# Kernel tuning notes

Hardware: AMD Instinct MI355X
Metric: run time of the kernel (lower is better)

The kernel has to match this reference:

```python
import jax, jax.numpy as jnp
import numpy as np

CROP = 20
HALF = CROP // 2  # also the zero-padding width
HID = 128
NCLS = 10
B = 16384


def setup_inputs() -> dict:
    key = jax.random.key(0)
    ks = jax.random.split(key, 16)
    s = 0.05
    inp = {
        "image": jax.random.uniform(ks[0], (B, 1, 28, 28), dtype=jnp.float32),
        # centers in padded coordinates, kept in-bounds: [HALF, 48-HALF]
        "center": jax.random.randint(ks[1], (B, 2), HALF, 48 - HALF + 1, dtype=jnp.int64),
        "h0": jax.random.normal(ks[2], (2, B, HID), dtype=jnp.float32),
        # RNN layer 0 (input 400 -> 128)
        "W_ih0": jax.random.normal(ks[3], (HID, CROP * CROP), dtype=jnp.float32) * s,
        "b_ih0": jax.random.normal(ks[4], (HID,), dtype=jnp.float32) * s,
        "W_hh0": jax.random.normal(ks[5], (HID, HID), dtype=jnp.float32) * s,
        "b_hh0": jax.random.normal(ks[6], (HID,), dtype=jnp.float32) * s,
        # RNN layer 1 (128 -> 128)
        "W_ih1": jax.random.normal(ks[7], (HID, HID), dtype=jnp.float32) * s,
        "b_ih1": jax.random.normal(ks[8], (HID,), dtype=jnp.float32) * s,
        "W_hh1": jax.random.normal(ks[9], (HID, HID), dtype=jnp.float32) * s,
        "b_hh1": jax.random.normal(ks[10], (HID,), dtype=jnp.float32) * s,
        # heads
        "W_cls": jax.random.normal(ks[11], (NCLS, HID), dtype=jnp.float32) * s,
        "b_cls": jax.random.normal(ks[12], (NCLS,), dtype=jnp.float32) * s,
        "W_act": jax.random.normal(ks[13], (2, HID), dtype=jnp.float32) * s,
        "b_act": jax.random.normal(ks[14], (2,), dtype=jnp.float32) * s,
    }
    return inp


def _crop(padded, center):
    # padded: (B,1,P,P), center: (B,2) with (x, y) in padded coords
    b = padded.shape[0]
    r = jnp.arange(CROP)
    ys = (center[:, 1] - HALF)[:, None] + r  # (B, CROP)
    xs = (center[:, 0] - HALF)[:, None] + r  # (B, CROP)
    bi = jnp.arange(b)[:, None, None]
    return padded[bi, 0, ys[:, :, None], xs[:, None, :]]  # (B, CROP, CROP)


def reference(image, center, h0,
              W_ih0, b_ih0, W_hh0, b_hh0,
              W_ih1, b_ih1, W_hh1, b_hh1,
              W_cls, b_cls, W_act, b_act):
    b = image.shape[0]
    padded = jnp.pad(image, ((0, 0), (0, 0), (HALF, HALF), (HALF, HALF)))
    x = _crop(padded, center).reshape(b, -1)  # (B, 400)
    # single-step, 2-layer tanh RNN
    h1 = jnp.tanh(x @ W_ih0.T + b_ih0 + h0[0] @ W_hh0.T + b_hh0)
    h2 = jnp.tanh(h1 @ W_ih1.T + b_ih1 + h0[1] @ W_hh1.T + b_hh1)
    hn = jnp.stack([h1, h2])  # (2, B, HID)
    class_pred = h2 @ W_cls.T + b_cls
    action_pred = h2 @ W_act.T + b_act
    return class_pred, action_pred, hn
```

## Files before the change

### kernel.cpp

```cpp
#include <hip/hip_runtime.h>
#include <hip/hip_bf16.h>

#define B_TOT 16384
#define MTILE 16

typedef __bf16 bf16x8 __attribute__((ext_vector_type(8)));
typedef float  f32x4  __attribute__((ext_vector_type(4)));

#define NG0 (17*8*64)
#define NG1 (8*8*64)
#define NGH (4*64)
#define WP0_OFF  0
#define WP1_OFF  (NG0*16)
#define WPH_OFF  (WP1_OFF + NG1*16)
#define BIAS0_OFF (WPH_OFF + NGH*16)
#define BIAS1_OFF (BIAS0_OFF + 512)
#define BIASH_OFF (BIAS1_OFF + 512)
#define ZERO_OFF  (BIASH_OFF + 512)
#define PREP_BLOCKS 53

__device__ __forceinline__ float fast_tanh(float x) {
    float cx = fminf(fmaxf(x, -9.f), 9.f);
    float t = __builtin_amdgcn_exp2f(cx * 2.8853900817779268f);
    return 1.f - 2.f * __builtin_amdgcn_rcpf(t + 1.f);
}

__device__ __forceinline__ void gl_lds4(const float* g, void* l) {
    __builtin_amdgcn_global_load_lds((const __attribute__((address_space(1))) void*)g,
                                     (__attribute__((address_space(3))) void*)l, 4, 0, 0);
}
__device__ __forceinline__ void gl_lds16(const float* g, void* l) {
    __builtin_amdgcn_global_load_lds((const __attribute__((address_space(1))) void*)g,
                                     (__attribute__((address_space(3))) void*)l, 16, 0, 0);
}

__device__ __forceinline__ bf16x8 cvt8(f32x4 a, f32x4 b) {
    bf16x8 v;
    v[0]=(__bf16)a.x; v[1]=(__bf16)a.y; v[2]=(__bf16)a.z; v[3]=(__bf16)a.w;
    v[4]=(__bf16)b.x; v[5]=(__bf16)b.y; v[6]=(__bf16)b.z; v[7]=(__bf16)b.w;
    return v;
}

__global__ __launch_bounds__(256) void prepack_kernel(
    const float* __restrict__ Wih0, const float* __restrict__ Whh0,
    const float* __restrict__ Wih1, const float* __restrict__ Whh1,
    const float* __restrict__ Wcls, const float* __restrict__ Wact,
    const float* __restrict__ bih0, const float* __restrict__ bhh0,
    const float* __restrict__ bih1, const float* __restrict__ bhh1,
    const float* __restrict__ bcls, const float* __restrict__ bact,
    char* __restrict__ ws)
{
    int idx = blockIdx.x * 256 + threadIdx.x;
    __bf16* wp0 = (__bf16*)(ws + WP0_OFF);
    __bf16* wp1 = (__bf16*)(ws + WP1_OFF);
    __bf16* wph = (__bf16*)(ws + WPH_OFF);
    float* bias0 = (float*)(ws + BIAS0_OFF);
    float* bias1 = (float*)(ws + BIAS1_OFF);
    float* biash = (float*)(ws + BIASH_OFF);

    if (idx < NG0) {
        int lane = idx & 63, g = idx >> 6, s = g >> 3, nb = g & 7;
        int n = nb * 16 + (lane & 15);
        int kb = s * 32 + (lane >> 4) * 8;
        bf16x8 v;
        #pragma unroll
        for (int j = 0; j < 8; ++j) {
            int k = kb + j;
            float x = 0.f;
            if (k < 400)       x = Wih0[n * 400 + k];
            else if (k >= 416) x = Whh0[n * 128 + (k - 416)];
            v[j] = (__bf16)x;
        }
        *(bf16x8*)(wp0 + (size_t)idx * 8) = v;
    } else if (idx < NG0 + NG1) {
        int i2 = idx - NG0;
        int lane = i2 & 63, g = i2 >> 6, s = g >> 3, nb = g & 7;
        int n = nb * 16 + (lane & 15);
        int kb = s * 32 + (lane >> 4) * 8;
        bf16x8 v;
        #pragma unroll
        for (int j = 0; j < 8; ++j) {
            int k = kb + j;
            float x = (k < 128) ? Wih1[n * 128 + k] : Whh1[n * 128 + (k - 128)];
            v[j] = (__bf16)x;
        }
        *(bf16x8*)(wp1 + (size_t)i2 * 8) = v;
    } else if (idx < NG0 + NG1 + NGH) {
        int i3 = idx - NG0 - NG1;
        int lane = i3 & 63, s = i3 >> 6;
        int n = lane & 15;
        int kb = s * 32 + (lane >> 4) * 8;
        bf16x8 v;
        #pragma unroll
        for (int j = 0; j < 8; ++j) {
            int k = kb + j;
            float x = 0.f;
            if (n < 10)      x = Wcls[n * 128 + k];
            else if (n < 12) x = Wact[(n - 10) * 128 + k];
            v[j] = (__bf16)x;
        }
        *(bf16x8*)(wph + (size_t)i3 * 8) = v;
    } else {
        int i4 = idx - NG0 - NG1 - NGH;
        if (i4 < 128) bias0[i4] = bih0[i4] + bhh0[i4];
        else if (i4 < 256) { int i = i4 - 128; bias1[i] = bih1[i] + bhh1[i]; }
        else if (i4 < 272) {
            int i = i4 - 256;
            biash[i] = (i < 10) ? bcls[i] : ((i < 12) ? bact[i - 10] : 0.f);
        } else if (i4 < 336) {
            ((float*)(ws + ZERO_OFF))[i4 - 272] = 0.f;
        }
    }
}

#define STGSTR 452
#define HEXSTR 136

__global__ __launch_bounds__(256) void fused_main(
    const float* __restrict__ image, const int* __restrict__ center,
    const float* __restrict__ h0, const char* __restrict__ ws,
    float* __restrict__ out)
{
    const bf16x8* wp0 = (const bf16x8*)(ws + WP0_OFF);
    const bf16x8* wp1 = (const bf16x8*)(ws + WP1_OFF);
    const bf16x8* wph = (const bf16x8*)(ws + WPH_OFF);
    const float* bias0 = (const float*)(ws + BIAS0_OFF);
    const float* bias1 = (const float*)(ws + BIAS1_OFF);
    const float* biash = (const float*)(ws + BIASH_OFF);
    const float* zbuf  = (const float*)(ws + ZERO_OFF);

    __shared__ __align__(16) float stage[MTILE * STGSTR];
    __shared__ __align__(16) float h0st[16 * 256];
    __shared__ __align__(16) __bf16 h1ex[MTILE * HEXSTR];
    __bf16* h2ex = (__bf16*)stage;

    const int t = threadIdx.x, lane = t & 63, wn = t >> 6;
    const int m0 = blockIdx.x * MTILE;
    const int l15 = lane & 15, l16 = lane >> 4;

    #pragma unroll
    for (int u = 0; u < 4; ++u) {
        int c = wn * 4 + u;
        int L = c >> 3, s = (c >> 1) & 3, half = c & 1;
        const float* src = h0 + (size_t)L * B_TOT * 128
                         + (size_t)(m0 + l15) * 128 + s * 32 + l16 * 8 + half * 4;
        gl_lds16(src, &h0st[c * 256]);
    }

    const int s0 = wn * 4;
    int cxv[4], cyv[4];
    #pragma unroll
    for (int i = 0; i < 4; ++i) {
        cxv[i] = center[(m0 + s0 + i) * 2 + 0];
        cyv[i] = center[(m0 + s0 + i) * 2 + 1];
    }

    {
        int k = lane;
        int r = k / 20, c = k - r * 20;
        #pragma unroll
        for (int j = 0; j < 7; ++j) {
            #pragma unroll
            for (int i = 0; i < 4; ++i) {
                int iy = cyv[i] - 20 + r;
                int ix = cxv[i] - 20 + c;
                bool ok = ((unsigned)iy < 28u) && ((unsigned)ix < 28u) && (k < 400);
                const float* src = ok ? (image + (size_t)(m0 + s0 + i) * 784 + iy * 28 + ix)
                                      : zbuf;
                gl_lds4(src, &stage[(s0 + i) * STGSTR + j * 64]);
            }
            k += 64;
            c += 4; if (c >= 20) { c -= 20; r += 4; } else { r += 3; }
        }
    }
    __syncthreads();

    const int cg = wn;
    const int qr = l16, lr = l15;
    const float* stg = stage + lr * STGSTR;

    float* outh1 = out + (size_t)B_TOT * 12;
    float* outh2 = out + (size_t)B_TOT * 140;

    f32x4 acc0[2] = {};
    #pragma unroll
    for (int s = 0; s < 13; ++s) {
        f32x4 fa = *(const f32x4*)(stg + s * 32 + qr * 8);
        f32x4 fb = *(const f32x4*)(stg + s * 32 + qr * 8 + 4);
        bf16x8 a = cvt8(fa, fb);
        bf16x8 b0 = wp0[(size_t)(s * 8 + cg * 2 + 0) * 64 + lane];
        bf16x8 b1 = wp0[(size_t)(s * 8 + cg * 2 + 1) * 64 + lane];
        acc0[0] = __builtin_amdgcn_mfma_f32_16x16x32_bf16(a, b0, acc0[0], 0, 0, 0);
        acc0[1] = __builtin_amdgcn_mfma_f32_16x16x32_bf16(a, b1, acc0[1], 0, 0, 0);
    }
    #pragma unroll
    for (int s = 0; s < 4; ++s) {
        f32x4 fa = *(const f32x4*)(h0st + (s * 2 + 0) * 256 + lane * 4);
        f32x4 fb = *(const f32x4*)(h0st + (s * 2 + 1) * 256 + lane * 4);
        bf16x8 a = cvt8(fa, fb);
        bf16x8 b0 = wp0[(size_t)((13 + s) * 8 + cg * 2 + 0) * 64 + lane];
        bf16x8 b1 = wp0[(size_t)((13 + s) * 8 + cg * 2 + 1) * 64 + lane];
        acc0[0] = __builtin_amdgcn_mfma_f32_16x16x32_bf16(a, b0, acc0[0], 0, 0, 0);
        acc0[1] = __builtin_amdgcn_mfma_f32_16x16x32_bf16(a, b1, acc0[1], 0, 0, 0);
    }
    #pragma unroll
    for (int f = 0; f < 2; ++f) {
        int n = cg * 32 + f * 16 + lr;
        float bv = bias0[n];
        #pragma unroll
        for (int r = 0; r < 4; ++r)
            h1ex[(qr * 4 + r) * HEXSTR + n] = (__bf16)fast_tanh(acc0[f][r] + bv);
    }

    f32x4 acc1[2] = {};
    #pragma unroll
    for (int s = 0; s < 4; ++s) {
        f32x4 fa = *(const f32x4*)(h0st + (8 + s * 2 + 0) * 256 + lane * 4);
        f32x4 fb = *(const f32x4*)(h0st + (8 + s * 2 + 1) * 256 + lane * 4);
        bf16x8 a = cvt8(fa, fb);
        bf16x8 b0 = wp1[(size_t)((4 + s) * 8 + cg * 2 + 0) * 64 + lane];
        bf16x8 b1 = wp1[(size_t)((4 + s) * 8 + cg * 2 + 1) * 64 + lane];
        acc1[0] = __builtin_amdgcn_mfma_f32_16x16x32_bf16(a, b0, acc1[0], 0, 0, 0);
        acc1[1] = __builtin_amdgcn_mfma_f32_16x16x32_bf16(a, b1, acc1[1], 0, 0, 0);
    }
    __syncthreads();

    {
        int row = t >> 4, c0 = (t & 15) * 8;
        bf16x8 hv = *(const bf16x8*)(h1ex + row * HEXSTR + c0);
        float4 o1, o2;
        o1.x=(float)hv[0]; o1.y=(float)hv[1]; o1.z=(float)hv[2]; o1.w=(float)hv[3];
        o2.x=(float)hv[4]; o2.y=(float)hv[5]; o2.z=(float)hv[6]; o2.w=(float)hv[7];
        *(float4*)(outh1 + (size_t)(m0 + row) * 128 + c0) = o1;
        *(float4*)(outh1 + (size_t)(m0 + row) * 128 + c0 + 4) = o2;
    }

    {
        const __bf16* h1row = h1ex + lr * HEXSTR + qr * 8;
        #pragma unroll
        for (int s = 0; s < 4; ++s) {
            bf16x8 a  = *(const bf16x8*)(h1row + s * 32);
            bf16x8 b0 = wp1[(size_t)(s * 8 + cg * 2 + 0) * 64 + lane];
            bf16x8 b1 = wp1[(size_t)(s * 8 + cg * 2 + 1) * 64 + lane];
            acc1[0] = __builtin_amdgcn_mfma_f32_16x16x32_bf16(a, b0, acc1[0], 0, 0, 0);
            acc1[1] = __builtin_amdgcn_mfma_f32_16x16x32_bf16(a, b1, acc1[1], 0, 0, 0);
        }
    }
    #pragma unroll
    for (int f = 0; f < 2; ++f) {
        int n = cg * 32 + f * 16 + lr;
        float bv = bias1[n];
        #pragma unroll
        for (int r = 0; r < 4; ++r)
            h2ex[(qr * 4 + r) * HEXSTR + n] = (__bf16)fast_tanh(acc1[f][r] + bv);
    }
    __syncthreads();

    {
        int row = t >> 4, c0 = (t & 15) * 8;
        bf16x8 hv = *(const bf16x8*)(h2ex + row * HEXSTR + c0);
        float4 o1, o2;
        o1.x=(float)hv[0]; o1.y=(float)hv[1]; o1.z=(float)hv[2]; o1.w=(float)hv[3];
        o2.x=(float)hv[4]; o2.y=(float)hv[5]; o2.z=(float)hv[6]; o2.w=(float)hv[7];
        *(float4*)(outh2 + (size_t)(m0 + row) * 128 + c0) = o1;
        *(float4*)(outh2 + (size_t)(m0 + row) * 128 + c0 + 4) = o2;
    }

    if (cg == 0) {
        f32x4 acc2 = {};
        const __bf16* h2row = h2ex + lr * HEXSTR + qr * 8;
        #pragma unroll
        for (int s = 0; s < 4; ++s) {
            bf16x8 a = *(const bf16x8*)(h2row + s * 32);
            bf16x8 b = wph[(size_t)s * 64 + lane];
            acc2 = __builtin_amdgcn_mfma_f32_16x16x32_bf16(a, b, acc2, 0, 0, 0);
        }
        float bhd = biash[lr];
        #pragma unroll
        for (int r = 0; r < 4; ++r) {
            int mg = m0 + qr * 4 + r;
            float v = acc2[r] + bhd;
            if (lr < 10)      out[(size_t)mg * 10 + lr] = v;
            else if (lr < 12) out[(size_t)B_TOT * 10 + (size_t)mg * 2 + (lr - 10)] = v;
        }
    }
}

extern "C" void kernel_launch(void* const* d_in, const int* in_sizes, int n_in,
                              void* d_out, int out_size, void* d_ws, size_t ws_size,
                              hipStream_t stream) {
    const float* image = (const float*)d_in[0];
    const int*   center = (const int*)d_in[1];
    const float* h0   = (const float*)d_in[2];
    const float* Wih0 = (const float*)d_in[3];
    const float* bih0 = (const float*)d_in[4];
    const float* Whh0 = (const float*)d_in[5];
    const float* bhh0 = (const float*)d_in[6];
    const float* Wih1 = (const float*)d_in[7];
    const float* bih1 = (const float*)d_in[8];
    const float* Whh1 = (const float*)d_in[9];
    const float* bhh1 = (const float*)d_in[10];
    const float* Wcls = (const float*)d_in[11];
    const float* bcls = (const float*)d_in[12];
    const float* Wact = (const float*)d_in[13];
    const float* bact = (const float*)d_in[14];

    prepack_kernel<<<PREP_BLOCKS, 256, 0, stream>>>(
        Wih0, Whh0, Wih1, Whh1, Wcls, Wact,
        bih0, bhh0, bih1, bhh1, bcls, bact, (char*)d_ws);
    fused_main<<<B_TOT / MTILE, 256, 0, stream>>>(
        image, center, h0, (const char*)d_ws, (float*)d_out);
}
```

Before: 29.08 us.

## Load contiguous image row band with 16B LDS DMA, then crop in LDS

Replaces the per-element 4-byte global-to-LDS gather of crop pixels with 16-byte loads of a contiguous 20-row band of each image into LDS. A second pass crops from that band, zero-pads and converts to bf16 in shared memory, so the MFMA loop reads bf16 directly. The h1/h2 outputs are now written in fp32 straight from the tanh results instead of via a bf16 LDS round trip, and the layer-1 h0 load is deferred to reuse LDS. This cuts the number of load instructions but adds an extra LDS pass, a barrier, and uncoalesced scalar output stores.

```diff
diff --git a/kernel.cpp b/kernel.cpp
--- a/kernel.cpp
+++ b/kernel.cpp
@@ -16,7 +16,6 @@
 #define BIAS0_OFF (WPH_OFF + NGH*16)
 #define BIAS1_OFF (BIAS0_OFF + 512)
 #define BIASH_OFF (BIAS1_OFF + 512)
-#define ZERO_OFF  (BIASH_OFF + 512)
 #define PREP_BLOCKS 53
 
 __device__ __forceinline__ float fast_tanh(float x) {
@@ -25,11 +24,7 @@
     return 1.f - 2.f * __builtin_amdgcn_rcpf(t + 1.f);
 }
 
-__device__ __forceinline__ void gl_lds4(const float* g, void* l) {
-    __builtin_amdgcn_global_load_lds((const __attribute__((address_space(1))) void*)g,
-                                     (__attribute__((address_space(3))) void*)l, 4, 0, 0);
-}
-__device__ __forceinline__ void gl_lds16(const float* g, void* l) {
+__device__ __forceinline__ void gl_lds16(const void* g, void* l) {
     __builtin_amdgcn_global_load_lds((const __attribute__((address_space(1))) void*)g,
                                      (__attribute__((address_space(3))) void*)l, 16, 0, 0);
 }
@@ -107,13 +102,12 @@
         else if (i4 < 272) {
             int i = i4 - 256;
             biash[i] = (i < 10) ? bcls[i] : ((i < 12) ? bact[i - 10] : 0.f);
-        } else if (i4 < 336) {
-            ((float*)(ws + ZERO_OFF))[i4 - 272] = 0.f;
-        }
-    }
-}
-
-#define STGSTR 452
+        }
+    }
+}
+
+#define RAWW  560
+#define XLSTR 424
 #define HEXSTR 136
 
 __global__ __launch_bounds__(256) void fused_main(
@@ -127,71 +121,107 @@
     const float* bias0 = (const float*)(ws + BIAS0_OFF);
     const float* bias1 = (const float*)(ws + BIAS1_OFF);
     const float* biash = (const float*)(ws + BIASH_OFF);
-    const float* zbuf  = (const float*)(ws + ZERO_OFF);
-
-    __shared__ __align__(16) float stage[MTILE * STGSTR];
-    __shared__ __align__(16) float h0st[16 * 256];
-    __shared__ __align__(16) __bf16 h1ex[MTILE * HEXSTR];
-    __bf16* h2ex = (__bf16*)stage;
+
+    __shared__ __align__(16) float raw[MTILE * RAWW];
+    __shared__ __align__(16) __bf16 stage[MTILE * XLSTR];
+    __shared__ __align__(16) float h0st[8 * 256];
+    __bf16* h1ex = (__bf16*)raw;
+    __bf16* h2ex = (__bf16*)(raw + 2048);
+    float*  h0st1 = raw + 4096;
 
     const int t = threadIdx.x, lane = t & 63, wn = t >> 6;
     const int m0 = blockIdx.x * MTILE;
     const int l15 = lane & 15, l16 = lane >> 4;
 
     #pragma unroll
-    for (int u = 0; u < 4; ++u) {
-        int c = wn * 4 + u;
-        int L = c >> 3, s = (c >> 1) & 3, half = c & 1;
-        const float* src = h0 + (size_t)L * B_TOT * 128
+    for (int u = 0; u < 2; ++u) {
+        int c = wn * 2 + u;
+        int s = c >> 1, half = c & 1;
+        const float* src = h0 + (size_t)(m0 + l15) * 128 + s * 32 + l16 * 8 + half * 4;
+        gl_lds16(src, &h0st[c * 256]);
+    }
+
+    {
+        unsigned basel = lane * 16u;
+        #pragma unroll
+        for (int j = 0; j < 9; ++j) {
+            int ii = wn + j * 4;
+            if (ii < 35) {
+                unsigned off = (unsigned)ii * 1024u + basel;
+                unsigned sm = off / 2240u;
+                unsigned within = off - sm * 2240u;
+                int cyl = center[(m0 + sm) * 2 + 1];
+                int rst = min(max(cyl - 20, 0), 8);
+                const char* src = (const char*)image
+                                + (size_t)(m0 + sm) * 3136 + (size_t)rst * 112 + within;
+                gl_lds16(src, (char*)raw + (size_t)ii * 1024);
+            }
+        }
+    }
+    __syncthreads();
+
+    {
+        int m = t >> 4, sub = t & 15;
+        int cyv = center[(m0 + m) * 2 + 1];
+        int cxv = center[(m0 + m) * 2 + 0];
+        int rst = min(max(cyv - 20, 0), 8);
+        const float* rawm = raw + m * RAWW;
+        __bf16* stm = stage + m * XLSTR;
+        #pragma unroll
+        for (int i = 0; i < 14; ++i) {
+            int k2 = (sub + i * 16) * 2;
+            if (k2 < XLSTR) {
+                float v0 = 0.f, v1 = 0.f;
+                if (k2 < 400) {
+                    int r0 = k2 / 20, c0 = k2 - r0 * 20;
+                    int iy = cyv - 20 + r0, ix = cxv - 20 + c0;
+                    bool ok = ((unsigned)iy < 28u) && ((unsigned)ix < 28u);
+                    int idx = ok ? ((iy - rst) * 28 + ix) : 0;
+                    float vv = rawm[idx];
+                    v0 = ok ? vv : 0.f;
+                    int k1 = k2 + 1;
+                    if (k1 < 400) {
+                        int r1 = (c0 == 19) ? r0 + 1 : r0;
+                        int c1 = (c0 == 19) ? 0 : c0 + 1;
+                        int iy1 = cyv - 20 + r1, ix1 = cxv - 20 + c1;
+                        bool ok1 = ((unsigned)iy1 < 28u) && ((unsigned)ix1 < 28u);
+                        int idx1 = ok1 ? ((iy1 - rst) * 28 + ix1) : 0;
+                        float vv1 = rawm[idx1];
+                        v1 = ok1 ? vv1 : 0.f;
+                    }
+                }
+                union { __bf16 b[2]; unsigned u; } p;
+                p.b[0] = (__bf16)v0; p.b[1] = (__bf16)v1;
+                *(unsigned*)(stm + k2) = p.u;
+            }
+        }
+    }
+    __syncthreads();
+
+    #pragma unroll
+    for (int u = 0; u < 2; ++u) {
+        int c = wn * 2 + u;
+        int s = c >> 1, half = c & 1;
+        const float* src = h0 + (size_t)B_TOT * 128
                          + (size_t)(m0 + l15) * 128 + s * 32 + l16 * 8 + half * 4;
-        gl_lds16(src, &h0st[c * 256]);
-    }
-
-    const int s0 = wn * 4;
-    int cxv[4], cyv[4];
-    #pragma unroll
-    for (int i = 0; i < 4; ++i) {
-        cxv[i] = center[(m0 + s0 + i) * 2 + 0];
-        cyv[i] = center[(m0 + s0 + i) * 2 + 1];
-    }
-
-    {
-        int k = lane;
-        int r = k / 20, c = k - r * 20;
-        #pragma unroll
-        for (int j = 0; j < 7; ++j) {
-            #pragma unroll
-            for (int i = 0; i < 4; ++i) {
-                int iy = cyv[i] - 20 + r;
-                int ix = cxv[i] - 20 + c;
-                bool ok = ((unsigned)iy < 28u) && ((unsigned)ix < 28u) && (k < 400);
-                const float* src = ok ? (image + (size_t)(m0 + s0 + i) * 784 + iy * 28 + ix)
-                                      : zbuf;
-                gl_lds4(src, &stage[(s0 + i) * STGSTR + j * 64]);
-            }
-            k += 64;
-            c += 4; if (c >= 20) { c -= 20; r += 4; } else { r += 3; }
-        }
-    }
-    __syncthreads();
-
-    const int cg = wn;
-    const int qr = l16, lr = l15;
-    const float* stg = stage + lr * STGSTR;
-
+        gl_lds16(src, &h0st1[c * 256]);
+    }
+
+    const int cg = wn, qr = l16, lr = l15;
     float* outh1 = out + (size_t)B_TOT * 12;
     float* outh2 = out + (size_t)B_TOT * 140;
 
     f32x4 acc0[2] = {};
-    #pragma unroll
-    for (int s = 0; s < 13; ++s) {
-        f32x4 fa = *(const f32x4*)(stg + s * 32 + qr * 8);
-        f32x4 fb = *(const f32x4*)(stg + s * 32 + qr * 8 + 4);
-        bf16x8 a = cvt8(fa, fb);
-        bf16x8 b0 = wp0[(size_t)(s * 8 + cg * 2 + 0) * 64 + lane];
-        bf16x8 b1 = wp0[(size_t)(s * 8 + cg * 2 + 1) * 64 + lane];
-        acc0[0] = __builtin_amdgcn_mfma_f32_16x16x32_bf16(a, b0, acc0[0], 0, 0, 0);
-        acc0[1] = __builtin_amdgcn_mfma_f32_16x16x32_bf16(a, b1, acc0[1], 0, 0, 0);
+    {
+        const __bf16* stg = stage + lr * XLSTR + qr * 8;
+        #pragma unroll
+        for (int s = 0; s < 13; ++s) {
+            bf16x8 a = *(const bf16x8*)(stg + s * 32);
+            bf16x8 b0 = wp0[(size_t)(s * 8 + cg * 2 + 0) * 64 + lane];
+            bf16x8 b1 = wp0[(size_t)(s * 8 + cg * 2 + 1) * 64 + lane];
+            acc0[0] = __builtin_amdgcn_mfma_f32_16x16x32_bf16(a, b0, acc0[0], 0, 0, 0);
+            acc0[1] = __builtin_amdgcn_mfma_f32_16x16x32_bf16(a, b1, acc0[1], 0, 0, 0);
+        }
     }
     #pragma unroll
     for (int s = 0; s < 4; ++s) {
@@ -208,33 +238,16 @@
         int n = cg * 32 + f * 16 + lr;
         float bv = bias0[n];
         #pragma unroll
-        for (int r = 0; r < 4; ++r)
-            h1ex[(qr * 4 + r) * HEXSTR + n] = (__bf16)fast_tanh(acc0[f][r] + bv);
-    }
+        for (int r = 0; r < 4; ++r) {
+            int ml = qr * 4 + r;
+            float hv = fast_tanh(acc0[f][r] + bv);
+            outh1[(size_t)(m0 + ml) * 128 + n] = hv;
+            h1ex[ml * HEXSTR + n] = (__bf16)hv;
+        }
+    }
+    __syncthreads();
 
     f32x4 acc1[2] = {};
-    #pragma unroll
-    for (int s = 0; s < 4; ++s) {
-        f32x4 fa = *(const f32x4*)(h0st + (8 + s * 2 + 0) * 256 + lane * 4);
-        f32x4 fb = *(const f32x4*)(h0st + (8 + s * 2 + 1) * 256 + lane * 4);
-        bf16x8 a = cvt8(fa, fb);
-        bf16x8 b0 = wp1[(size_t)((4 + s) * 8 + cg * 2 + 0) * 64 + lane];
-        bf16x8 b1 = wp1[(size_t)((4 + s) * 8 + cg * 2 + 1) * 64 + lane];
-        acc1[0] = __builtin_amdgcn_mfma_f32_16x16x32_bf16(a, b0, acc1[0], 0, 0, 0);
-        acc1[1] = __builtin_amdgcn_mfma_f32_16x16x32_bf16(a, b1, acc1[1], 0, 0, 0);
-    }
-    __syncthreads();
-
-    {
-        int row = t >> 4, c0 = (t & 15) * 8;
-        bf16x8 hv = *(const bf16x8*)(h1ex + row * HEXSTR + c0);
-        float4 o1, o2;
-        o1.x=(float)hv[0]; o1.y=(float)hv[1]; o1.z=(float)hv[2]; o1.w=(float)hv[3];
-        o2.x=(float)hv[4]; o2.y=(float)hv[5]; o2.z=(float)hv[6]; o2.w=(float)hv[7];
-        *(float4*)(outh1 + (size_t)(m0 + row) * 128 + c0) = o1;
-        *(float4*)(outh1 + (size_t)(m0 + row) * 128 + c0 + 4) = o2;
-    }
-
     {
         const __bf16* h1row = h1ex + lr * HEXSTR + qr * 8;
         #pragma unroll
@@ -247,24 +260,28 @@
         }
     }
     #pragma unroll
+    for (int s = 0; s < 4; ++s) {
+        f32x4 fa = *(const f32x4*)(h0st1 + (s * 2 + 0) * 256 + lane * 4);
+        f32x4 fb = *(const f32x4*)(h0st1 + (s * 2 + 1) * 256 + lane * 4);
+        bf16x8 a = cvt8(fa, fb);
+        bf16x8 b0 = wp1[(size_t)((4 + s) * 8 + cg * 2 + 0) * 64 + lane];
+        bf16x8 b1 = wp1[(size_t)((4 + s) * 8 + cg * 2 + 1) * 64 + lane];
+        acc1[0] = __builtin_amdgcn_mfma_f32_16x16x32_bf16(a, b0, acc1[0], 0, 0, 0);
+        acc1[1] = __builtin_amdgcn_mfma_f32_16x16x32_bf16(a, b1, acc1[1], 0, 0, 0);
+    }
+    #pragma unroll
     for (int f = 0; f < 2; ++f) {
         int n = cg * 32 + f * 16 + lr;
         float bv = bias1[n];
         #pragma unroll
-        for (int r = 0; r < 4; ++r)
-            h2ex[(qr * 4 + r) * HEXSTR + n] = (__bf16)fast_tanh(acc1[f][r] + bv);
+        for (int r = 0; r < 4; ++r) {
+            int ml = qr * 4 + r;
+            float hv = fast_tanh(acc1[f][r] + bv);
+            outh2[(size_t)(m0 + ml) * 128 + n] = hv;
+            h2ex[ml * HEXSTR + n] = (__bf16)hv;
+        }
     }
     __syncthreads();
-
-    {
-        int row = t >> 4, c0 = (t & 15) * 8;
-        bf16x8 hv = *(const bf16x8*)(h2ex + row * HEXSTR + c0);
-        float4 o1, o2;
-        o1.x=(float)hv[0]; o1.y=(float)hv[1]; o1.z=(float)hv[2]; o1.w=(float)hv[3];
-        o2.x=(float)hv[4]; o2.y=(float)hv[5]; o2.z=(float)hv[6]; o2.w=(float)hv[7];
-        *(float4*)(outh2 + (size_t)(m0 + row) * 128 + c0) = o1;
-        *(float4*)(outh2 + (size_t)(m0 + row) * 128 + c0 + 4) = o2;
-    }
 
     if (cg == 0) {
         f32x4 acc2 = {};
```

Result: slower. 33.24 us (+14.3%).

## Load h0 directly from global and write hidden states straight from MFMA registers

Applied to the files above, without the earlier changes.

Drops the LDS staging buffer for h0. Each lane now loads its h0 fragment from global memory just before the recurrent MFMAs. The bf16 round-trip through LDS for the h1/h2 output stores is replaced by scattered fp32 stores straight from the tanh results. This cuts LDS footprint, so more blocks may fit per CU, and outputs keep full fp32 precision instead of bf16-rounded values. The cost is uncoalesced scalar global stores with a 16-element column stride, and h0 global-load latency that is no longer hidden behind the crop loads.

```diff
diff --git a/kernel.cpp b/kernel.cpp
--- a/kernel.cpp
+++ b/kernel.cpp
@@ -28,10 +28,6 @@
 __device__ __forceinline__ void gl_lds4(const float* g, void* l) {
     __builtin_amdgcn_global_load_lds((const __attribute__((address_space(1))) void*)g,
                                      (__attribute__((address_space(3))) void*)l, 4, 0, 0);
-}
-__device__ __forceinline__ void gl_lds16(const float* g, void* l) {
-    __builtin_amdgcn_global_load_lds((const __attribute__((address_space(1))) void*)g,
-                                     (__attribute__((address_space(3))) void*)l, 16, 0, 0);
 }
 
 __device__ __forceinline__ bf16x8 cvt8(f32x4 a, f32x4 b) {
@@ -130,22 +126,12 @@
     const float* zbuf  = (const float*)(ws + ZERO_OFF);
 
     __shared__ __align__(16) float stage[MTILE * STGSTR];
-    __shared__ __align__(16) float h0st[16 * 256];
     __shared__ __align__(16) __bf16 h1ex[MTILE * HEXSTR];
     __bf16* h2ex = (__bf16*)stage;
 
     const int t = threadIdx.x, lane = t & 63, wn = t >> 6;
     const int m0 = blockIdx.x * MTILE;
     const int l15 = lane & 15, l16 = lane >> 4;
-
-    #pragma unroll
-    for (int u = 0; u < 4; ++u) {
-        int c = wn * 4 + u;
-        int L = c >> 3, s = (c >> 1) & 3, half = c & 1;
-        const float* src = h0 + (size_t)L * B_TOT * 128
-                         + (size_t)(m0 + l15) * 128 + s * 32 + l16 * 8 + half * 4;
-        gl_lds16(src, &h0st[c * 256]);
-    }
 
     const int s0 = wn * 4;
     int cxv[4], cyv[4];
@@ -178,6 +164,8 @@
     const int cg = wn;
     const int qr = l16, lr = l15;
     const float* stg = stage + lr * STGSTR;
+    const float* h0r0 = h0 + (size_t)(m0 + lr) * 128 + qr * 8;
+    const float* h0r1 = h0r0 + (size_t)B_TOT * 128;
 
     float* outh1 = out + (size_t)B_TOT * 12;
     float* outh2 = out + (size_t)B_TOT * 140;
@@ -195,8 +183,8 @@
     }
     #pragma unroll
     for (int s = 0; s < 4; ++s) {
-        f32x4 fa = *(const f32x4*)(h0st + (s * 2 + 0) * 256 + lane * 4);
-        f32x4 fb = *(const f32x4*)(h0st + (s * 2 + 1) * 256 + lane * 4);
+        f32x4 fa = *(const f32x4*)(h0r0 + s * 32);
+        f32x4 fb = *(const f32x4*)(h0r0 + s * 32 + 4);
         bf16x8 a = cvt8(fa, fb);
         bf16x8 b0 = wp0[(size_t)((13 + s) * 8 + cg * 2 + 0) * 64 + lane];
         bf16x8 b1 = wp0[(size_t)((13 + s) * 8 + cg * 2 + 1) * 64 + lane];
@@ -208,15 +196,19 @@
         int n = cg * 32 + f * 16 + lr;
         float bv = bias0[n];
         #pragma unroll
-        for (int r = 0; r < 4; ++r)
-            h1ex[(qr * 4 + r) * HEXSTR + n] = (__bf16)fast_tanh(acc0[f][r] + bv);
+        for (int r = 0; r < 4; ++r) {
+            int ml = qr * 4 + r;
+            float hv = fast_tanh(acc0[f][r] + bv);
+            outh1[(size_t)(m0 + ml) * 128 + n] = hv;
+            h1ex[ml * HEXSTR + n] = (__bf16)hv;
+        }
     }
 
     f32x4 acc1[2] = {};
     #pragma unroll
     for (int s = 0; s < 4; ++s) {
-        f32x4 fa = *(const f32x4*)(h0st + (8 + s * 2 + 0) * 256 + lane * 4);
-        f32x4 fb = *(const f32x4*)(h0st + (8 + s * 2 + 1) * 256 + lane * 4);
+        f32x4 fa = *(const f32x4*)(h0r1 + s * 32);
+        f32x4 fb = *(const f32x4*)(h0r1 + s * 32 + 4);
         bf16x8 a = cvt8(fa, fb);
         bf16x8 b0 = wp1[(size_t)((4 + s) * 8 + cg * 2 + 0) * 64 + lane];
         bf16x8 b1 = wp1[(size_t)((4 + s) * 8 + cg * 2 + 1) * 64 + lane];
@@ -224,16 +216,6 @@
         acc1[1] = __builtin_amdgcn_mfma_f32_16x16x32_bf16(a, b1, acc1[1], 0, 0, 0);
     }
     __syncthreads();
-
-    {
-        int row = t >> 4, c0 = (t & 15) * 8;
-        bf16x8 hv = *(const bf16x8*)(h1ex + row * HEXSTR + c0);
-        float4 o1, o2;
-        o1.x=(float)hv[0]; o1.y=(float)hv[1]; o1.z=(float)hv[2]; o1.w=(float)hv[3];
-        o2.x=(float)hv[4]; o2.y=(float)hv[5]; o2.z=(float)hv[6]; o2.w=(float)hv[7];
-        *(float4*)(outh1 + (size_t)(m0 + row) * 128 + c0) = o1;
-        *(float4*)(outh1 + (size_t)(m0 + row) * 128 + c0 + 4) = o2;
-    }
 
     {
         const __bf16* h1row = h1ex + lr * HEXSTR + qr * 8;
@@ -251,20 +233,14 @@
         int n = cg * 32 + f * 16 + lr;
         float bv = bias1[n];
         #pragma unroll
-        for (int r = 0; r < 4; ++r)
-            h2ex[(qr * 4 + r) * HEXSTR + n] = (__bf16)fast_tanh(acc1[f][r] + bv);
+        for (int r = 0; r < 4; ++r) {
+            int ml = qr * 4 + r;
+            float hv = fast_tanh(acc1[f][r] + bv);
+            outh2[(size_t)(m0 + ml) * 128 + n] = hv;
+            h2ex[ml * HEXSTR + n] = (__bf16)hv;
+        }
     }
     __syncthreads();
-
-    {
-        int row = t >> 4, c0 = (t & 15) * 8;
-        bf16x8 hv = *(const bf16x8*)(h2ex + row * HEXSTR + c0);
-        float4 o1, o2;
-        o1.x=(float)hv[0]; o1.y=(float)hv[1]; o1.z=(float)hv[2]; o1.w=(float)hv[3];
-        o2.x=(float)hv[4]; o2.y=(float)hv[5]; o2.z=(float)hv[6]; o2.w=(float)hv[7];
-        *(float4*)(outh2 + (size_t)(m0 + row) * 128 + c0) = o1;
-        *(float4*)(outh2 + (size_t)(m0 + row) * 128 + c0 + 4) = o2;
-    }
 
     if (cg == 0) {
         f32x4 acc2 = {};
```

Result: slower. 32.22 us (+10.8%).

## Stream weight fragments through per-wave LDS ring with async global-to-LDS loads

Applied to the files above, without the earlier changes.

Weight fragments that were loaded straight from global memory into registers are now prefetched into a per-wave 6-slot LDS ring using global_load_lds. Explicit vmcnt/lgkmcnt waits keep four fragments in flight ahead of the MFMA chain. The aim is to hide weight-load latency behind the matrix math. Biases are also loaded early, and the h1 and h2 output stores are merged after a single barrier, which delays the h1 writeback. The hand-written waitcnt and sched barriers constrain the compiler's scheduling, and the ring adds LDS use that may lower occupancy.

```diff
diff --git a/kernel.cpp b/kernel.cpp
--- a/kernel.cpp
+++ b/kernel.cpp
@@ -29,7 +29,7 @@
     __builtin_amdgcn_global_load_lds((const __attribute__((address_space(1))) void*)g,
                                      (__attribute__((address_space(3))) void*)l, 4, 0, 0);
 }
-__device__ __forceinline__ void gl_lds16(const float* g, void* l) {
+__device__ __forceinline__ void gl_lds16(const void* g, void* l) {
     __builtin_amdgcn_global_load_lds((const __attribute__((address_space(1))) void*)g,
                                      (__attribute__((address_space(3))) void*)l, 16, 0, 0);
 }
@@ -115,28 +115,48 @@
 
 #define STGSTR 452
 #define HEXSTR 136
+#define RSLOTS 6
+
+#define RWAIT(n) do { asm volatile("s_waitcnt vmcnt(" #n ")" ::: "memory"); \
+                      __builtin_amdgcn_sched_barrier(0); } while (0)
+#define LFENCE   do { asm volatile("s_waitcnt lgkmcnt(0)" ::: "memory"); \
+                      __builtin_amdgcn_sched_barrier(0); } while (0)
+
+__device__ __forceinline__ void issue_fi(int fi, const char* wp0b, const char* wp1b,
+                                         int cg, char* ringw, int lane) {
+    int s = fi >> 1, half = fi & 1;
+    int frag; const char* base;
+    if (s < 17)      { base = wp0b; frag = s * 8 + cg * 2 + half; }
+    else if (s < 21) { base = wp1b; frag = (4 + (s - 17)) * 8 + cg * 2 + half; }
+    else             { base = wp1b; frag = (s - 21) * 8 + cg * 2 + half; }
+    gl_lds16(base + (size_t)frag * 1024 + (size_t)lane * 16,
+             ringw + (size_t)(fi % RSLOTS) * 1024);
+}
 
 __global__ __launch_bounds__(256) void fused_main(
     const float* __restrict__ image, const int* __restrict__ center,
     const float* __restrict__ h0, const char* __restrict__ ws,
     float* __restrict__ out)
 {
-    const bf16x8* wp0 = (const bf16x8*)(ws + WP0_OFF);
-    const bf16x8* wp1 = (const bf16x8*)(ws + WP1_OFF);
-    const bf16x8* wph = (const bf16x8*)(ws + WPH_OFF);
     const float* bias0 = (const float*)(ws + BIAS0_OFF);
     const float* bias1 = (const float*)(ws + BIAS1_OFF);
     const float* biash = (const float*)(ws + BIASH_OFF);
     const float* zbuf  = (const float*)(ws + ZERO_OFF);
+    const char* wp0b = ws + WP0_OFF;
+    const char* wp1b = ws + WP1_OFF;
+    const bf16x8* wph = (const bf16x8*)(ws + WPH_OFF);
 
     __shared__ __align__(16) float stage[MTILE * STGSTR];
     __shared__ __align__(16) float h0st[16 * 256];
     __shared__ __align__(16) __bf16 h1ex[MTILE * HEXSTR];
+    __shared__ __align__(16) __bf16 ringb[4 * RSLOTS * 512];
     __bf16* h2ex = (__bf16*)stage;
 
     const int t = threadIdx.x, lane = t & 63, wn = t >> 6;
     const int m0 = blockIdx.x * MTILE;
     const int l15 = lane & 15, l16 = lane >> 4;
+    const int cg = wn, qr = l16, lr = l15;
+    char* ringw = (char*)ringb + (size_t)wn * (RSLOTS * 1024);
 
     #pragma unroll
     for (int u = 0; u < 4; ++u) {
@@ -154,6 +174,8 @@
         cxv[i] = center[(m0 + s0 + i) * 2 + 0];
         cyv[i] = center[(m0 + s0 + i) * 2 + 1];
     }
+    const float bv00 = bias0[cg * 32 + lr],      bv01 = bias0[cg * 32 + 16 + lr];
+    const float bv10 = bias1[cg * 32 + lr],      bv11 = bias1[cg * 32 + 16 + lr];
 
     {
         int k = lane;
@@ -175,95 +197,134 @@
     }
     __syncthreads();
 
-    const int cg = wn;
-    const int qr = l16, lr = l15;
     const float* stg = stage + lr * STGSTR;
+    f32x4 acc0[2] = {}, acc1[2] = {};
+
+    issue_fi(0, wp0b, wp1b, cg, ringw, lane);
+    issue_fi(1, wp0b, wp1b, cg, ringw, lane);
+    issue_fi(2, wp0b, wp1b, cg, ringw, lane);
+    issue_fi(3, wp0b, wp1b, cg, ringw, lane);
+
+    #pragma unroll
+    for (int s = 0; s < 13; ++s) {
+        RWAIT(2);
+        f32x4 fa = *(const f32x4*)(stg + s * 32 + qr * 8);
+        f32x4 fb = *(const f32x4*)(stg + s * 32 + qr * 8 + 4);
+        bf16x8 b0 = *(const bf16x8*)(ringw + (size_t)((2 * s) % RSLOTS) * 1024 + (size_t)lane * 16);
+        bf16x8 b1 = *(const bf16x8*)(ringw + (size_t)((2 * s + 1) % RSLOTS) * 1024 + (size_t)lane * 16);
+        LFENCE;
+        issue_fi(2 * s + 4, wp0b, wp1b, cg, ringw, lane);
+        issue_fi(2 * s + 5, wp0b, wp1b, cg, ringw, lane);
+        bf16x8 a = cvt8(fa, fb);
+        acc0[0] = __builtin_amdgcn_mfma_f32_16x16x32_bf16(a, b0, acc0[0], 0, 0, 0);
+        acc0[1] = __builtin_amdgcn_mfma_f32_16x16x32_bf16(a, b1, acc0[1], 0, 0, 0);
+    }
+    #pragma unroll
+    for (int u = 0; u < 4; ++u) {
+        const int s = 13 + u;
+        RWAIT(2);
+        f32x4 fa = *(const f32x4*)(h0st + (u * 2 + 0) * 256 + lane * 4);
+        f32x4 fb = *(const f32x4*)(h0st + (u * 2 + 1) * 256 + lane * 4);
+        bf16x8 b0 = *(const bf16x8*)(ringw + (size_t)((2 * s) % RSLOTS) * 1024 + (size_t)lane * 16);
+        bf16x8 b1 = *(const bf16x8*)(ringw + (size_t)((2 * s + 1) % RSLOTS) * 1024 + (size_t)lane * 16);
+        LFENCE;
+        issue_fi(2 * s + 4, wp0b, wp1b, cg, ringw, lane);
+        issue_fi(2 * s + 5, wp0b, wp1b, cg, ringw, lane);
+        bf16x8 a = cvt8(fa, fb);
+        acc0[0] = __builtin_amdgcn_mfma_f32_16x16x32_bf16(a, b0, acc0[0], 0, 0, 0);
+        acc0[1] = __builtin_amdgcn_mfma_f32_16x16x32_bf16(a, b1, acc0[1], 0, 0, 0);
+    }
+    #pragma unroll
+    for (int r = 0; r < 4; ++r) {
+        int ml = qr * 4 + r;
+        h1ex[ml * HEXSTR + cg * 32 + lr]      = (__bf16)fast_tanh(acc0[0][r] + bv00);
+        h1ex[ml * HEXSTR + cg * 32 + 16 + lr] = (__bf16)fast_tanh(acc0[1][r] + bv01);
+    }
+    #pragma unroll
+    for (int u = 0; u < 4; ++u) {
+        const int s = 17 + u;
+        RWAIT(2);
+        f32x4 fa = *(const f32x4*)(h0st + (8 + u * 2 + 0) * 256 + lane * 4);
+        f32x4 fb = *(const f32x4*)(h0st + (8 + u * 2 + 1) * 256 + lane * 4);
+        bf16x8 b0 = *(const bf16x8*)(ringw + (size_t)((2 * s) % RSLOTS) * 1024 + (size_t)lane * 16);
+        bf16x8 b1 = *(const bf16x8*)(ringw + (size_t)((2 * s + 1) % RSLOTS) * 1024 + (size_t)lane * 16);
+        LFENCE;
+        if (s < 20) {
+            issue_fi(2 * s + 4, wp0b, wp1b, cg, ringw, lane);
+            issue_fi(2 * s + 5, wp0b, wp1b, cg, ringw, lane);
+        } else {
+            issue_fi(44, wp0b, wp1b, cg, ringw, lane);
+            issue_fi(45, wp0b, wp1b, cg, ringw, lane);
+        }
+        bf16x8 a = cvt8(fa, fb);
+        acc1[0] = __builtin_amdgcn_mfma_f32_16x16x32_bf16(a, b0, acc1[0], 0, 0, 0);
+        acc1[1] = __builtin_amdgcn_mfma_f32_16x16x32_bf16(a, b1, acc1[1], 0, 0, 0);
+    }
+    __syncthreads();
+
+    {
+        const __bf16* h1row = h1ex + lr * HEXSTR + qr * 8;
+        {
+            bf16x8 a = *(const bf16x8*)(h1row + 0 * 32);
+            bf16x8 b0 = *(const bf16x8*)(ringw + (size_t)(42 % RSLOTS) * 1024 + (size_t)lane * 16);
+            bf16x8 b1 = *(const bf16x8*)(ringw + (size_t)(43 % RSLOTS) * 1024 + (size_t)lane * 16);
+            LFENCE;
+            issue_fi(46, wp0b, wp1b, cg, ringw, lane);
+            issue_fi(47, wp0b, wp1b, cg, ringw, lane);
+            acc1[0] = __builtin_amdgcn_mfma_f32_16x16x32_bf16(a, b0, acc1[0], 0, 0, 0);
+            acc1[1] = __builtin_amdgcn_mfma_f32_16x16x32_bf16(a, b1, acc1[1], 0, 0, 0);
+        }
+        {
+            bf16x8 a = *(const bf16x8*)(h1row + 1 * 32);
+            bf16x8 b0 = *(const bf16x8*)(ringw + (size_t)(44 % RSLOTS) * 1024 + (size_t)lane * 16);
+            bf16x8 b1 = *(const bf16x8*)(ringw + (size_t)(45 % RSLOTS) * 1024 + (size_t)lane * 16);
+            LFENCE;
+            issue_fi(48, wp0b, wp1b, cg, ringw, lane);
+            issue_fi(49, wp0b, wp1b, cg, ringw, lane);
+            acc1[0] = __builtin_amdgcn_mfma_f32_16x16x32_bf16(a, b0, acc1[0], 0, 0, 0);
+            acc1[1] = __builtin_amdgcn_mfma_f32_16x16x32_bf16(a, b1, acc1[1], 0, 0, 0);
+        }
+        RWAIT(2);
+        {
+            bf16x8 a = *(const bf16x8*)(h1row + 2 * 32);
+            bf16x8 b0 = *(const bf16x8*)(ringw + (size_t)(46 % RSLOTS) * 1024 + (size_t)lane * 16);
+            bf16x8 b1 = *(const bf16x8*)(ringw + (size_t)(47 % RSLOTS) * 1024 + (size_t)lane * 16);
+            acc1[0] = __builtin_amdgcn_mfma_f32_16x16x32_bf16(a, b0, acc1[0], 0, 0, 0);
+            acc1[1] = __builtin_amdgcn_mfma_f32_16x16x32_bf16(a, b1, acc1[1], 0, 0, 0);
+        }
+        RWAIT(0);
+        {
+            bf16x8 a = *(const bf16x8*)(h1row + 3 * 32);
+            bf16x8 b0 = *(const bf16x8*)(ringw + (size_t)(48 % RSLOTS) * 1024 + (size_t)lane * 16);
+            bf16x8 b1 = *(const bf16x8*)(ringw + (size_t)(49 % RSLOTS) * 1024 + (size_t)lane * 16);
+            acc1[0] = __builtin_amdgcn_mfma_f32_16x16x32_bf16(a, b0, acc1[0], 0, 0, 0);
+            acc1[1] = __builtin_amdgcn_mfma_f32_16x16x32_bf16(a, b1, acc1[1], 0, 0, 0);
+        }
+    }
+    #pragma unroll
+    for (int r = 0; r < 4; ++r) {
+        int ml = qr * 4 + r;
+        h2ex[ml * HEXSTR + cg * 32 + lr]      = (__bf16)fast_tanh(acc1[0][r] + bv10);
+        h2ex[ml * HEXSTR + cg * 32 + 16 + lr] = (__bf16)fast_tanh(acc1[1][r] + bv11);
+    }
+    __syncthreads();
 
     float* outh1 = out + (size_t)B_TOT * 12;
     float* outh2 = out + (size_t)B_TOT * 140;
 
-    f32x4 acc0[2] = {};
-    #pragma unroll
-    for (int s = 0; s < 13; ++s) {
-        f32x4 fa = *(const f32x4*)(stg + s * 32 + qr * 8);
-        f32x4 fb = *(const f32x4*)(stg + s * 32 + qr * 8 + 4);
-        bf16x8 a = cvt8(fa, fb);
-        bf16x8 b0 = wp0[(size_t)(s * 8 + cg * 2 + 0) * 64 + lane];
-        bf16x8 b1 = wp0[(size_t)(s * 8 + cg * 2 + 1) * 64 + lane];
-        acc0[0] = __builtin_amdgcn_mfma_f32_16x16x32_bf16(a, b0, acc0[0], 0, 0, 0);
-        acc0[1] = __builtin_amdgcn_mfma_f32_16x16x32_bf16(a, b1, acc0[1], 0, 0, 0);
-    }
-    #pragma unroll
-    for (int s = 0; s < 4; ++s) {
-        f32x4 fa = *(const f32x4*)(h0st + (s * 2 + 0) * 256 + lane * 4);
-        f32x4 fb = *(const f32x4*)(h0st + (s * 2 + 1) * 256 + lane * 4);
-        bf16x8 a = cvt8(fa, fb);
-        bf16x8 b0 = wp0[(size_t)((13 + s) * 8 + cg * 2 + 0) * 64 + lane];
-        bf16x8 b1 = wp0[(size_t)((13 + s) * 8 + cg * 2 + 1) * 64 + lane];
-        acc0[0] = __builtin_amdgcn_mfma_f32_16x16x32_bf16(a, b0, acc0[0], 0, 0, 0);
-        acc0[1] = __builtin_amdgcn_mfma_f32_16x16x32_bf16(a, b1, acc0[1], 0, 0, 0);
-    }
-    #pragma unroll
-    for (int f = 0; f < 2; ++f) {
-        int n = cg * 32 + f * 16 + lr;
-        float bv = bias0[n];
-        #pragma unroll
-        for (int r = 0; r < 4; ++r)
-            h1ex[(qr * 4 + r) * HEXSTR + n] = (__bf16)fast_tanh(acc0[f][r] + bv);
-    }
-
-    f32x4 acc1[2] = {};
-    #pragma unroll
-    for (int s = 0; s < 4; ++s) {
-        f32x4 fa = *(const f32x4*)(h0st + (8 + s * 2 + 0) * 256 + lane * 4);
-        f32x4 fb = *(const f32x4*)(h0st + (8 + s * 2 + 1) * 256 + lane * 4);
-        bf16x8 a = cvt8(fa, fb);
-        bf16x8 b0 = wp1[(size_t)((4 + s) * 8 + cg * 2 + 0) * 64 + lane];
-        bf16x8 b1 = wp1[(size_t)((4 + s) * 8 + cg * 2 + 1) * 64 + lane];
-        acc1[0] = __builtin_amdgcn_mfma_f32_16x16x32_bf16(a, b0, acc1[0], 0, 0, 0);
-        acc1[1] = __builtin_amdgcn_mfma_f32_16x16x32_bf16(a, b1, acc1[1], 0, 0, 0);
-    }
-    __syncthreads();
-
     {
         int row = t >> 4, c0 = (t & 15) * 8;
-        bf16x8 hv = *(const bf16x8*)(h1ex + row * HEXSTR + c0);
-        float4 o1, o2;
-        o1.x=(float)hv[0]; o1.y=(float)hv[1]; o1.z=(float)hv[2]; o1.w=(float)hv[3];
-        o2.x=(float)hv[4]; o2.y=(float)hv[5]; o2.z=(float)hv[6]; o2.w=(float)hv[7];
-        *(float4*)(outh1 + (size_t)(m0 + row) * 128 + c0) = o1;
+        bf16x8 hv1 = *(const bf16x8*)(h1ex + row * HEXSTR + c0);
+        bf16x8 hv2 = *(const bf16x8*)(h2ex + row * HEXSTR + c0);
+        float4 o1, o2, o3, o4;
+        o1.x=(float)hv1[0]; o1.y=(float)hv1[1]; o1.z=(float)hv1[2]; o1.w=(float)hv1[3];
+        o2.x=(float)hv1[4]; o2.y=(float)hv1[5]; o2.z=(float)hv1[6]; o2.w=(float)hv1[7];
+        o3.x=(float)hv2[0]; o3.y=(float)hv2[1]; o3.z=(float)hv2[2]; o3.w=(float)hv2[3];
+        o4.x=(float)hv2[4]; o4.y=(float)hv2[5]; o4.z=(float)hv2[6]; o4.w=(float)hv2[7];
+        *(float4*)(outh1 + (size_t)(m0 + row) * 128 + c0)     = o1;
         *(float4*)(outh1 + (size_t)(m0 + row) * 128 + c0 + 4) = o2;
-    }
-
-    {
-        const __bf16* h1row = h1ex + lr * HEXSTR + qr * 8;
-        #pragma unroll
-        for (int s = 0; s < 4; ++s) {
-            bf16x8 a  = *(const bf16x8*)(h1row + s * 32);
-            bf16x8 b0 = wp1[(size_t)(s * 8 + cg * 2 + 0) * 64 + lane];
-            bf16x8 b1 = wp1[(size_t)(s * 8 + cg * 2 + 1) * 64 + lane];
-            acc1[0] = __builtin_amdgcn_mfma_f32_16x16x32_bf16(a, b0, acc1[0], 0, 0, 0);
-            acc1[1] = __builtin_amdgcn_mfma_f32_16x16x32_bf16(a, b1, acc1[1], 0, 0, 0);
-        }
-    }
-    #pragma unroll
-    for (int f = 0; f < 2; ++f) {
-        int n = cg * 32 + f * 16 + lr;
-        float bv = bias1[n];
-        #pragma unroll
-        for (int r = 0; r < 4; ++r)
-            h2ex[(qr * 4 + r) * HEXSTR + n] = (__bf16)fast_tanh(acc1[f][r] + bv);
-    }
-    __syncthreads();
-
-    {
-        int row = t >> 4, c0 = (t & 15) * 8;
-        bf16x8 hv = *(const bf16x8*)(h2ex + row * HEXSTR + c0);
-        float4 o1, o2;
-        o1.x=(float)hv[0]; o1.y=(float)hv[1]; o1.z=(float)hv[2]; o1.w=(float)hv[3];
-        o2.x=(float)hv[4]; o2.y=(float)hv[5]; o2.z=(float)hv[6]; o2.w=(float)hv[7];
-        *(float4*)(outh2 + (size_t)(m0 + row) * 128 + c0) = o1;
-        *(float4*)(outh2 + (size_t)(m0 + row) * 128 + c0 + 4) = o2;
+        *(float4*)(outh2 + (size_t)(m0 + row) * 128 + c0)     = o3;
+        *(float4*)(outh2 + (size_t)(m0 + row) * 128 + c0 + 4) = o4;
     }
 
     if (cg == 0) {
```

After: 34.91 us. +20.1%, slower.
